# Optimization experiments

Measured on AMD Instinct MI355X. Metric: run time of the kernel, lower is better.

Reference implementation:

```python
import jax, jax.numpy as jnp
import numpy as np

B, S, D, H, DK, DV = 4, 2048, 512, 8, 64, 64
LN_EPS = 1e-5


def setup_inputs() -> dict:
    key = jax.random.key(0)
    ks = jax.random.split(key, 8)
    scale = 1.0 / np.sqrt(D)
    return {
        "input_Q": jax.random.normal(ks[0], (B, S, D), jnp.float32),
        "input_K": jax.random.normal(ks[1], (B, S, D), jnp.float32),
        "input_V": jax.random.normal(ks[2], (B, S, D), jnp.float32),
        "attn_mask": jax.random.randint(ks[3], (B, S, S), 0, 2).astype(jnp.bool_),
        "W_Q": jax.random.normal(ks[4], (D, H * DK), jnp.float32) * scale,
        "W_K": jax.random.normal(ks[5], (D, H * DK), jnp.float32) * scale,
        "W_V": jax.random.normal(ks[6], (D, H * DV), jnp.float32) * scale,
        "W_fc": jax.random.normal(ks[7], (H * DV, D), jnp.float32) * scale,
        "ln_gamma": jnp.ones((D,), jnp.float32),
        "ln_beta": jnp.zeros((D,), jnp.float32),
    }


def reference(input_Q, input_K, input_V, attn_mask, W_Q, W_K, W_V, W_fc, ln_gamma, ln_beta):
    b, s, _ = input_Q.shape
    # projections -> [b, h, s, d]
    Q = (input_Q @ W_Q).reshape(b, s, H, DK).transpose(0, 2, 1, 3)
    K = (input_K @ W_K).reshape(b, s, H, DK).transpose(0, 2, 1, 3)
    V = (input_V @ W_V).reshape(b, s, H, DV).transpose(0, 2, 1, 3)
    # full [b, h, q, k] score matrix (faithful to explicit matmul->mask->softmax)
    scores = jnp.einsum("bhqd,bhkd->bhqk", Q, K) / np.sqrt(DK).astype(np.float32)
    scores = jnp.where(attn_mask[:, None, :, :], -jnp.inf, scores)
    attn = jax.nn.softmax(scores, axis=-1)
    context = jnp.einsum("bhqk,bhkd->bhqd", attn, V)  # [b, h, s, dv]
    context = context.transpose(0, 2, 1, 3).reshape(b, s, H * DV)
    output = context @ W_fc  # dropout is identity in eval / p=0
    x = output + input_Q  # residual
    mean = jnp.mean(x, axis=-1, keepdims=True)
    var = jnp.var(x, axis=-1, keepdims=True)
    return (x - mean) * jax.lax.rsqrt(var + LN_EPS) * ln_gamma + ln_beta
```

## Files before the change

### kernel.cpp

```cpp
#include <hip/hip_runtime.h>


#define B_ 4
#define S_ 2048
#define D_ 512
#define H_ 8

typedef __attribute__((ext_vector_type(8))) short short8_t;
typedef __attribute__((ext_vector_type(4))) short short4_t;
typedef __attribute__((ext_vector_type(4))) float f32x4;
typedef __attribute__((ext_vector_type(16))) float f32x16;
typedef __attribute__((ext_vector_type(4))) unsigned u32x4;
typedef __attribute__((ext_vector_type(2))) unsigned u32x2;

__device__ __forceinline__ short f2bf(float f) {
    unsigned u = __builtin_bit_cast(unsigned, f);
    u += 0x7fff + ((u >> 16) & 1);
    return (short)(u >> 16);
}

__device__ __forceinline__ unsigned pk2(float a, float b) {
    return __builtin_amdgcn_perm(__builtin_bit_cast(unsigned, b),
                                 __builtin_bit_cast(unsigned, a), 0x07060302u);
}

__device__ __forceinline__ float bflo(unsigned u) {
    return __builtin_bit_cast(float, u << 16);
}
__device__ __forceinline__ float bfhi(unsigned u) {
    return __builtin_bit_cast(float, u & 0xffff0000u);
}

__global__ __launch_bounds__(256) void pack_mask_kernel(const void* __restrict__ mask,
                                                        unsigned* __restrict__ bits) {
    __shared__ int isBool;
    if (threadIdx.x == 0) isBool = 0;
    __syncthreads();
    const unsigned char* bytes = (const unsigned char*)mask;
    if (threadIdx.x < 64) {
        if (bytes[threadIdx.x * 4 + 1] | bytes[threadIdx.x * 4 + 2] | bytes[threadIdx.x * 4 + 3])
            isBool = 1;
    }
    __syncthreads();
    int t = blockIdx.x * 256 + threadIdx.x;
    int half = t & 1, q = (t >> 1) & 2047, kt = (t >> 12) & 31, b = t >> 17;
    size_t src = ((size_t)(b * 2048 + q)) * 2048 + kt * 64 + half * 32;
    unsigned v = 0;
    if (isBool) {
        const unsigned char* p = bytes + src;
        #pragma unroll
        for (int i = 0; i < 32; ++i) v |= (p[i] ? 1u : 0u) << i;
    } else {
        const int* p = (const int*)mask + src;
        #pragma unroll
        for (int i = 0; i < 32; ++i) v |= (p[i] ? 1u : 0u) << i;
    }
    bits[(((size_t)(b * 32 + kt)) * 2048 + q) * 2 + half] = ~v;
}

__global__ __launch_bounds__(256) void proj_kernel(
    const float* __restrict__ inQ, const float* __restrict__ inK, const float* __restrict__ inV,
    const float* __restrict__ wq, const float* __restrict__ wk, const float* __restrict__ wv,
    short* __restrict__ Qp, short* __restrict__ Kp, short* __restrict__ Vp) {
    __shared__ short As[64 * 64];
    __shared__ short Bs[64 * 64];
    const int z = blockIdx.z;
    const float* A = (z == 0) ? inQ : ((z == 1) ? inK : inV);
    const float* W = (z == 0) ? wq : ((z == 1) ? wk : wv);
    short* O = (z == 0) ? Qp : ((z == 1) ? Kp : Vp);
    const float scale = (z == 0) ? 0.125f * 1.44269504f : 1.0f;
    const int bm = blockIdx.x * 64, bn = blockIdx.y * 64;
    const int tid = threadIdx.x, lane = tid & 63, wv_ = tid >> 6;
    const int wm = (wv_ >> 1) * 32, wn = (wv_ & 1) * 32;
    f32x4 acc[2][2] = {};

    for (int k0 = 0; k0 < 512; k0 += 64) {
        __syncthreads();
        #pragma unroll
        for (int it = 0; it < 4; ++it) {
            int g = tid + it * 256;
            int r = g >> 4, c4 = (g & 15) * 4;
            f32x4 v = *(const f32x4*)(A + (size_t)(bm + r) * 512 + k0 + c4);
            u32x2 u = { pk2(v.x, v.y), pk2(v.z, v.w) };
            *(u32x2*)((char*)As + r * 128 + ((c4 * 2) ^ ((r & 7) << 4))) = u;
        }
        #pragma unroll
        for (int it = 0; it < 2; ++it) {
            int g = tid + it * 256;
            int kp = g >> 4, n4 = (g & 15) * 4;
            const float* wrow = W + (size_t)(k0 + 2 * kp) * 512 + bn + n4;
            f32x4 va = *(const f32x4*)(wrow);
            f32x4 vb = *(const f32x4*)(wrow + 512);
            #pragma unroll
            for (int j = 0; j < 4; ++j) {
                int n = n4 + j;
                *(unsigned*)((char*)Bs + n * 128 + ((4 * kp) ^ ((n & 7) << 4))) = pk2(va[j], vb[j]);
            }
        }
        __syncthreads();
        #pragma unroll
        for (int kk = 0; kk < 2; ++kk) {
            short8_t af[2], bfr[2];
            #pragma unroll
            for (int rf = 0; rf < 2; ++rf) {
                int row = wm + rf * 16 + (lane & 15);
                af[rf] = *(const short8_t*)((const char*)As + row * 128 +
                          ((kk * 64 + ((lane >> 4) * 16)) ^ ((row & 7) << 4)));
            }
            #pragma unroll
            for (int cf = 0; cf < 2; ++cf) {
                int n = wn + cf * 16 + (lane & 15);
                bfr[cf] = *(const short8_t*)((const char*)Bs + n * 128 +
                           ((kk * 64 + ((lane >> 4) * 16)) ^ ((n & 7) << 4)));
            }
            __builtin_amdgcn_s_setprio(1);
            #pragma unroll
            for (int rf = 0; rf < 2; ++rf)
                #pragma unroll
                for (int cf = 0; cf < 2; ++cf)
                    acc[rf][cf] = __builtin_amdgcn_mfma_f32_16x16x32_bf16(af[rf], bfr[cf], acc[rf][cf], 0, 0, 0);
            __builtin_amdgcn_s_setprio(0);
        }
    }

    if (z == 0) {
        #pragma unroll
        for (int rf = 0; rf < 2; ++rf)
            #pragma unroll
            for (int cf = 0; cf < 2; ++cf)
                #pragma unroll
                for (int r = 0; r < 4; ++r) {
                    int row = bm + wm + rf * 16 + (lane >> 4) * 4 + r;
                    int col = bn + wn + cf * 16 + (lane & 15);
                    size_t idx = ((((size_t)(row >> 11)) * 8 + (col >> 6)) * 2048 + (row & 2047)) * 64 + (col & 63);
                    O[idx] = f2bf(acc[rf][cf][r] * scale);
                }
    } else {
        const int bb = bm >> 11, kt = (bm & 2047) >> 6, hh = bn >> 6;
        const size_t base = ((size_t)(bb * 8 + hh)) * 131072 + (size_t)kt * 4096;
        __syncthreads();
        if (z == 1) {
            #pragma unroll
            for (int rf = 0; rf < 2; ++rf)
                #pragma unroll
                for (int cf = 0; cf < 2; ++cf)
                    #pragma unroll
                    for (int r = 0; r < 4; ++r) {
                        int key = wm + rf * 16 + (lane >> 4) * 4 + r;
                        int dk = wn + cf * 16 + (lane & 15);
                        *(short*)((char*)As + key * 128 + ((dk * 2) ^ ((key & 7) << 4))) = f2bf(acc[rf][cf][r]);
                    }
        } else {
            #pragma unroll
            for (int rf = 0; rf < 2; ++rf)
                #pragma unroll
                for (int cf = 0; cf < 2; ++cf)
                    #pragma unroll
                    for (int r = 0; r < 4; ++r) {
                        int key = wm + rf * 16 + (lane >> 4) * 4 + r;
                        int dv = wn + cf * 16 + (lane & 15);
                        *(short*)((char*)As + dv * 128 + ((key * 2) ^ ((dv & 7) << 4))) = f2bf(acc[rf][cf][r]);
                    }
        }
        __syncthreads();
        #pragma unroll
        for (int it = 0; it < 2; ++it) {
            int u = tid + it * 256;
            int blk = u >> 7, h2 = (u >> 6) & 1, rr = u & 63;
            short8_t v8 = *(const short8_t*)((const char*)As + rr * 128 +
                           ((blk * 32 + h2 * 16) ^ ((rr & 7) << 4)));
            *(short8_t*)(O + base + (size_t)u * 8) = v8;
        }
    }
}

template<int NSPLIT>
__global__ __launch_bounds__(256, 4) void attn_kernel(
    const short* __restrict__ Qp, const short* __restrict__ Kf, const short* __restrict__ Vf,
    const unsigned long long* __restrict__ mbits64, short* __restrict__ ctx,
    short* __restrict__ pO, float* __restrict__ pL) {
    __shared__ short Pw_all[4][2048];
    int flat = blockIdx.x + 16 * (blockIdx.y + 8 * NSPLIT * blockIdx.z);
    int x8 = flat & 7, s = flat >> 3;
    int group = x8 * (4 * NSPLIT) + (s >> 4);
    int qi = s & 15;
    int bh = group / NSPLIT, kvh = group % NSPLIT;
    const int b = bh >> 3, h = bh & 7;
    const int tid = threadIdx.x, lane = tid & 63, w = tid >> 6;
    const int hi = lane >> 5, r31 = lane & 31;
    const size_t hb = ((size_t)(b * 8 + h)) * 131072;
    const int qw = qi * 128 + w * 32;
    const int q_lane = qw + r31;
    const int NT = 32 / NSPLIT;
    const int t_beg = kvh * NT, t_end = t_beg + NT;

    short8_t qf[4];
    #pragma unroll
    for (int ks = 0; ks < 4; ++ks)
        qf[ks] = *(const short8_t*)(Qp + hb + (size_t)q_lane * 64 + ks * 16 + hi * 8);

    const short* Kb_ = Kf + hb + hi * 512 + r31 * 8;
    const short* Vb_ = Vf + hb + hi * 512 + r31 * 8;
    const unsigned long long* mrow = mbits64 + (size_t)b * 65536 + q_lane;

    f32x16 o0 = {}, o1 = {};
    float l_run = 0.f;

    for (int kt = t_beg; kt < t_end; ++kt) {
        const short* kp = Kb_ + (size_t)kt * 4096;
        unsigned long long wmx = mrow[(size_t)kt * 2048] >> (hi * 4);
        unsigned kl = (unsigned)wmx, kh = (unsigned)(wmx >> 32);

        f32x16 s0 = {}, s1 = {};
        __builtin_amdgcn_s_setprio(1);
        #pragma unroll
        for (int ks = 0; ks < 4; ++ks) {
            short8_t kf0 = *(const short8_t*)(kp + ks * 1024);
            short8_t kf1 = *(const short8_t*)(kp + ks * 1024 + 256);
            s0 = __builtin_amdgcn_mfma_f32_32x32x16_bf16(kf0, qf[ks], s0, 0, 0, 0);
            s1 = __builtin_amdgcn_mfma_f32_32x32x16_bf16(kf1, qf[ks], s1, 0, 0, 0);
        }
        __builtin_amdgcn_s_setprio(0);

        float r4[4] = { 0.f, 0.f, 0.f, 0.f };
        #pragma unroll
        for (int reg = 0; reg < 16; ++reg) {
            const int pos = (reg >> 2) * 8 + (reg & 3);
            float e0 = __builtin_amdgcn_exp2f(s0[reg]);
            float e1 = __builtin_amdgcn_exp2f(s1[reg]);
            unsigned k0b = (unsigned)__builtin_amdgcn_sbfe((int)kl, pos, 1);
            unsigned k1b = (unsigned)__builtin_amdgcn_sbfe((int)kh, pos, 1);
            float v0 = __builtin_bit_cast(float, __builtin_bit_cast(unsigned, e0) & k0b);
            float v1 = __builtin_bit_cast(float, __builtin_bit_cast(unsigned, e1) & k1b);
            s0[reg] = v0; s1[reg] = v1;
            r4[reg & 3] += v0 + v1;
        }
        float rs = (r4[0] + r4[1]) + (r4[2] + r4[3]);
        rs += __shfl_xor(rs, 32, 64);
        l_run += rs;

        const short* vp = Vb_ + (size_t)kt * 4096;
        #pragma unroll
        for (int kb = 0; kb < 4; ++kb) {
            const int e = (kb & 1) * 8;
            unsigned c0 = (kb < 2) ? pk2(s0[e + 0], s0[e + 1]) : pk2(s1[e + 0], s1[e + 1]);
            unsigned c1 = (kb < 2) ? pk2(s0[e + 2], s0[e + 3]) : pk2(s1[e + 2], s1[e + 3]);
            unsigned c2 = (kb < 2) ? pk2(s0[e + 4], s0[e + 5]) : pk2(s1[e + 4], s1[e + 5]);
            unsigned c3 = (kb < 2) ? pk2(s0[e + 6], s0[e + 7]) : pk2(s1[e + 6], s1[e + 7]);
#if __has_builtin(__builtin_amdgcn_permlane32_swap)
            u32x2 r02 = __builtin_amdgcn_permlane32_swap(c0, c2, false, false);
            u32x2 r13 = __builtin_amdgcn_permlane32_swap(c1, c3, false, false);
            u32x4 bw = { r02[0], r13[0], r02[1], r13[1] };
#else
            unsigned x0 = __shfl_xor(c0, 32, 64), x1 = __shfl_xor(c1, 32, 64);
            unsigned x2 = __shfl_xor(c2, 32, 64), x3 = __shfl_xor(c3, 32, 64);
            unsigned w0 = hi ? x2 : c0, w1 = hi ? x3 : c1;
            unsigned w2 = hi ? c2 : x0, w3 = hi ? c3 : x1;
            u32x4 bw = { w0, w1, w2, w3 };
#endif
            short8_t pb = __builtin_bit_cast(short8_t, bw);
            short8_t vf0 = *(const short8_t*)(vp + kb * 1024);
            short8_t vf1 = *(const short8_t*)(vp + kb * 1024 + 256);
            __builtin_amdgcn_s_setprio(1);
            o0 = __builtin_amdgcn_mfma_f32_32x32x16_bf16(vf0, pb, o0, 0, 0, 0);
            o1 = __builtin_amdgcn_mfma_f32_32x32x16_bf16(vf1, pb, o1, 0, 0, 0);
            __builtin_amdgcn_s_setprio(0);
        }
    }

    float invl = 1.0f / fmaxf(l_run, 1e-37f);
    short* Pw = Pw_all[w];
    #pragma unroll
    for (int dvb = 0; dvb < 2; ++dvb)
        #pragma unroll
        for (int g = 0; g < 4; ++g) {
            short4_t v4;
            #pragma unroll
            for (int t = 0; t < 4; ++t) {
                float val = (dvb ? o1[g * 4 + t] : o0[g * 4 + t]) * invl;
                v4[t] = f2bf(val);
            }
            int dv0 = dvb * 32 + g * 8 + hi * 4;
            *(short4_t*)((char*)Pw + r31 * 128 + ((dv0 * 2) ^ ((r31 & 7) << 4))) = v4;
        }
    asm volatile("s_waitcnt lgkmcnt(0)" ::: "memory");
    if (NSPLIT > 1) {
        const size_t bhn = (size_t)(bh * NSPLIT + kvh);
        #pragma unroll
        for (int c = 0; c < 4; ++c) {
            int idx = c * 64 + lane;
            int qq = idx >> 3, ch = idx & 7;
            short8_t rowv = *(const short8_t*)((const char*)Pw + qq * 128 + ((ch * 16) ^ ((qq & 7) << 4)));
            *(short8_t*)(pO + (bhn * 2048 + qw + qq) * 64 + ch * 8) = rowv;
        }
        if (lane < 32) pL[bhn * 2048 + q_lane] = l_run;
    } else {
        #pragma unroll
        for (int c = 0; c < 4; ++c) {
            int idx = c * 64 + lane;
            int qq = idx >> 3, ch = idx & 7;
            short8_t rowv = *(const short8_t*)((const char*)Pw + qq * 128 + ((ch * 16) ^ ((qq & 7) << 4)));
            *(short8_t*)(ctx + ((size_t)(b * 2048 + qw + qq)) * 512 + h * 64 + ch * 8) = rowv;
        }
    }
}

template<int NSPLIT>
__global__ __launch_bounds__(256) void combine_kernel(
    const short* __restrict__ pO, const float* __restrict__ pL,
    short* __restrict__ ctx) {
    const int row = blockIdx.x;
    const int b = row >> 11, q = row & 2047;
    const int e0 = threadIdx.x * 2;
    const int h = e0 >> 6, dv = e0 & 63;
    const size_t base = ((size_t)((b * 8 + h) * NSPLIT)) * 2048 + q;
    float wsum = 0.f, r0 = 0.f, r1 = 0.f;
    #pragma unroll
    for (int i = 0; i < NSPLIT; ++i) {
        float wv = pL[base + (size_t)i * 2048];
        unsigned a = *(const unsigned*)(pO + (base + (size_t)i * 2048) * 64 + dv);
        wsum += wv;
        r0 += bflo(a) * wv;
        r1 += bfhi(a) * wv;
    }
    float inv = 1.f / fmaxf(wsum, 1e-37f);
    *(unsigned*)(ctx + (size_t)row * 512 + e0) = pk2(r0 * inv, r1 * inv);
}

__global__ __launch_bounds__(256) void fc_kernel(
    const short* __restrict__ ctx, const float* __restrict__ wfc,
    const float* __restrict__ inQ, float* __restrict__ xbuf) {
    __shared__ short As[64 * 64];
    __shared__ short Bs[64 * 64];
    const int bm = blockIdx.x * 64, bn = blockIdx.y * 64;
    const int tid = threadIdx.x, lane = tid & 63, wv_ = tid >> 6;
    const int wm = (wv_ >> 1) * 32, wn = (wv_ & 1) * 32;
    f32x4 acc[2][2] = {};

    for (int k0 = 0; k0 < 512; k0 += 64) {
        __syncthreads();
        #pragma unroll
        for (int it = 0; it < 2; ++it) {
            int g = tid + it * 256;
            int r = g >> 3, c8 = (g & 7) * 8;
            short8_t v = *(const short8_t*)(ctx + (size_t)(bm + r) * 512 + k0 + c8);
            *(short8_t*)((char*)As + r * 128 + ((c8 * 2) ^ ((r & 7) << 4))) = v;
        }
        #pragma unroll
        for (int it = 0; it < 2; ++it) {
            int g = tid + it * 256;
            int kp = g >> 4, n4 = (g & 15) * 4;
            const float* wrow = wfc + (size_t)(k0 + 2 * kp) * 512 + bn + n4;
            f32x4 va = *(const f32x4*)(wrow);
            f32x4 vb = *(const f32x4*)(wrow + 512);
            #pragma unroll
            for (int j = 0; j < 4; ++j) {
                int n = n4 + j;
                *(unsigned*)((char*)Bs + n * 128 + ((4 * kp) ^ ((n & 7) << 4))) = pk2(va[j], vb[j]);
            }
        }
        __syncthreads();
        #pragma unroll
        for (int kk = 0; kk < 2; ++kk) {
            short8_t af[2], bfr[2];
            #pragma unroll
            for (int rf = 0; rf < 2; ++rf) {
                int row = wm + rf * 16 + (lane & 15);
                af[rf] = *(const short8_t*)((const char*)As + row * 128 +
                          ((kk * 64 + ((lane >> 4) * 16)) ^ ((row & 7) << 4)));
            }
            #pragma unroll
            for (int cf = 0; cf < 2; ++cf) {
                int n = wn + cf * 16 + (lane & 15);
                bfr[cf] = *(const short8_t*)((const char*)Bs + n * 128 +
                           ((kk * 64 + ((lane >> 4) * 16)) ^ ((n & 7) << 4)));
            }
            __builtin_amdgcn_s_setprio(1);
            #pragma unroll
            for (int rf = 0; rf < 2; ++rf)
                #pragma unroll
                for (int cf = 0; cf < 2; ++cf)
                    acc[rf][cf] = __builtin_amdgcn_mfma_f32_16x16x32_bf16(af[rf], bfr[cf], acc[rf][cf], 0, 0, 0);
            __builtin_amdgcn_s_setprio(0);
        }
    }
    #pragma unroll
    for (int rf = 0; rf < 2; ++rf)
        #pragma unroll
        for (int cf = 0; cf < 2; ++cf)
            #pragma unroll
            for (int r = 0; r < 4; ++r) {
                int row = bm + wm + rf * 16 + (lane >> 4) * 4 + r;
                int col = bn + wn + cf * 16 + (lane & 15);
                size_t idx = (size_t)row * 512 + col;
                xbuf[idx] = acc[rf][cf][r] + inQ[idx];
            }
}

__global__ __launch_bounds__(256) void ln_kernel(
    const float* __restrict__ x, const float* __restrict__ gamma,
    const float* __restrict__ beta, float* __restrict__ out) {
    __shared__ float rs[4], rq[4];
    const int row = blockIdx.x, tid = threadIdx.x;
    const int w = tid >> 6, lane = tid & 63;
    float2 v = *(const float2*)(x + (size_t)row * 512 + tid * 2);
    float s = v.x + v.y, sq = v.x * v.x + v.y * v.y;
    #pragma unroll
    for (int off = 32; off; off >>= 1) {
        s += __shfl_down(s, off, 64);
        sq += __shfl_down(sq, off, 64);
    }
    if (lane == 0) { rs[w] = s; rq[w] = sq; }
    __syncthreads();
    if (tid == 0) {
        rs[0] = rs[0] + rs[1] + rs[2] + rs[3];
        rq[0] = rq[0] + rq[1] + rq[2] + rq[3];
    }
    __syncthreads();
    float mean = rs[0] * (1.f / 512.f);
    float var = rq[0] * (1.f / 512.f) - mean * mean;
    float inv = rsqrtf(var + 1e-5f);
    int c0 = tid * 2;
    float2 g = *(const float2*)(gamma + c0);
    float2 be = *(const float2*)(beta + c0);
    float2 o;
    o.x = (v.x - mean) * inv * g.x + be.x;
    o.y = (v.y - mean) * inv * g.y + be.y;
    *(float2*)(out + (size_t)row * 512 + c0) = o;
}

extern "C" void kernel_launch(void* const* d_in, const int* in_sizes, int n_in,
                              void* d_out, int out_size, void* d_ws, size_t ws_size,
                              hipStream_t stream) {
    const float* inQ = (const float*)d_in[0];
    const float* inK = (const float*)d_in[1];
    const float* inV = (const float*)d_in[2];
    const void* mask = d_in[3];
    const float* wq = (const float*)d_in[4];
    const float* wk = (const float*)d_in[5];
    const float* wv = (const float*)d_in[6];
    const float* wfc = (const float*)d_in[7];
    const float* gamma = (const float*)d_in[8];
    const float* beta = (const float*)d_in[9];
    float* out = (float*)d_out;
    char* ws = (char*)d_ws;

    short* Qp = (short*)(ws);
    short* Kp = (short*)(ws + (size_t)(8 << 20));
    short* Vp = (short*)(ws + (size_t)(16 << 20));
    short* ctx = (short*)(ws + (size_t)(24 << 20));
    unsigned* mbits = (unsigned*)(ws + (size_t)(32 << 20));
    float* xbuf = (float*)(ws);

    short* pO = (short*)(ws + 35651584ull);
    float* pL = (float*)(ws + 35651584ull + 16777216ull);

    const bool split2 = ws_size >= 53477376ull;

    pack_mask_kernel<<<2048, 256, 0, stream>>>(mask, mbits);
    proj_kernel<<<dim3(128, 8, 3), 256, 0, stream>>>(inQ, inK, inV, wq, wk, wv, Qp, Kp, Vp);
    if (split2) {
        attn_kernel<2><<<dim3(16, 16, 4), 256, 0, stream>>>(
            Qp, Kp, Vp, (const unsigned long long*)mbits, ctx, pO, pL);
        combine_kernel<2><<<8192, 256, 0, stream>>>(pO, pL, ctx);
    } else {
        attn_kernel<1><<<dim3(16, 8, 4), 256, 0, stream>>>(
            Qp, Kp, Vp, (const unsigned long long*)mbits, ctx, pO, pL);
    }
    fc_kernel<<<dim3(128, 8, 1), 256, 0, stream>>>(ctx, wfc, inQ, xbuf);
    ln_kernel<<<8192, 256, 0, stream>>>(xbuf, gamma, beta, out);
}
```

Before: 142.8 us.

## Split KV across waves within block and combine in LDS, drop combine kernel

Each attention block now handles 32 queries, and its four waves each process a quarter of the key tiles. The wave results are merged in shared memory using the per-row softmax sums. This removes the separate global split-KV pass (partial output writes, the combine kernel launch and its re-reads) and gives more blocks. In exchange each block reloads Q per wave, gets less K/V reuse across queries, and adds a block-wide barrier plus an LDS reduction.

```diff
diff --git a/kernel.cpp b/kernel.cpp
--- a/kernel.cpp
+++ b/kernel.cpp
@@ -24,11 +24,8 @@
                                  __builtin_bit_cast(unsigned, a), 0x07060302u);
 }
 
-__device__ __forceinline__ float bflo(unsigned u) {
-    return __builtin_bit_cast(float, u << 16);
-}
-__device__ __forceinline__ float bfhi(unsigned u) {
-    return __builtin_bit_cast(float, u & 0xffff0000u);
+__device__ __forceinline__ float bf2f(short v) {
+    return __builtin_bit_cast(float, (unsigned)((unsigned short)v) << 16);
 }
 
 __global__ __launch_bounds__(256) void pack_mask_kernel(const void* __restrict__ mask,
@@ -174,25 +171,22 @@
     }
 }
 
-template<int NSPLIT>
 __global__ __launch_bounds__(256, 4) void attn_kernel(
     const short* __restrict__ Qp, const short* __restrict__ Kf, const short* __restrict__ Vf,
-    const unsigned long long* __restrict__ mbits64, short* __restrict__ ctx,
-    short* __restrict__ pO, float* __restrict__ pL) {
+    const unsigned long long* __restrict__ mbits64, short* __restrict__ ctx) {
     __shared__ short Pw_all[4][2048];
-    int flat = blockIdx.x + 16 * (blockIdx.y + 8 * NSPLIT * blockIdx.z);
+    __shared__ float l_lds[4][32];
+    int flat = blockIdx.x + 64 * (blockIdx.y + 8 * blockIdx.z);
     int x8 = flat & 7, s = flat >> 3;
-    int group = x8 * (4 * NSPLIT) + (s >> 4);
-    int qi = s & 15;
-    int bh = group / NSPLIT, kvh = group % NSPLIT;
+    int bh = x8 * 4 + (s >> 6);
+    int qi = s & 63;
     const int b = bh >> 3, h = bh & 7;
     const int tid = threadIdx.x, lane = tid & 63, w = tid >> 6;
     const int hi = lane >> 5, r31 = lane & 31;
-    const size_t hb = ((size_t)(b * 8 + h)) * 131072;
-    const int qw = qi * 128 + w * 32;
+    const size_t hb = ((size_t)bh) * 131072;
+    const int qw = qi * 32;
     const int q_lane = qw + r31;
-    const int NT = 32 / NSPLIT;
-    const int t_beg = kvh * NT, t_end = t_beg + NT;
+    const int t_beg = w * 8, t_end = t_beg + 8;
 
     short8_t qf[4];
     #pragma unroll
@@ -283,48 +277,26 @@
             int dv0 = dvb * 32 + g * 8 + hi * 4;
             *(short4_t*)((char*)Pw + r31 * 128 + ((dv0 * 2) ^ ((r31 & 7) << 4))) = v4;
         }
-    asm volatile("s_waitcnt lgkmcnt(0)" ::: "memory");
-    if (NSPLIT > 1) {
-        const size_t bhn = (size_t)(bh * NSPLIT + kvh);
-        #pragma unroll
-        for (int c = 0; c < 4; ++c) {
-            int idx = c * 64 + lane;
-            int qq = idx >> 3, ch = idx & 7;
-            short8_t rowv = *(const short8_t*)((const char*)Pw + qq * 128 + ((ch * 16) ^ ((qq & 7) << 4)));
-            *(short8_t*)(pO + (bhn * 2048 + qw + qq) * 64 + ch * 8) = rowv;
-        }
-        if (lane < 32) pL[bhn * 2048 + q_lane] = l_run;
-    } else {
-        #pragma unroll
-        for (int c = 0; c < 4; ++c) {
-            int idx = c * 64 + lane;
-            int qq = idx >> 3, ch = idx & 7;
-            short8_t rowv = *(const short8_t*)((const char*)Pw + qq * 128 + ((ch * 16) ^ ((qq & 7) << 4)));
-            *(short8_t*)(ctx + ((size_t)(b * 2048 + qw + qq)) * 512 + h * 64 + ch * 8) = rowv;
-        }
-    }
-}
-
-template<int NSPLIT>
-__global__ __launch_bounds__(256) void combine_kernel(
-    const short* __restrict__ pO, const float* __restrict__ pL,
-    short* __restrict__ ctx) {
-    const int row = blockIdx.x;
-    const int b = row >> 11, q = row & 2047;
-    const int e0 = threadIdx.x * 2;
-    const int h = e0 >> 6, dv = e0 & 63;
-    const size_t base = ((size_t)((b * 8 + h) * NSPLIT)) * 2048 + q;
-    float wsum = 0.f, r0 = 0.f, r1 = 0.f;
+    if (hi == 0) l_lds[w][r31] = l_run;
+    __syncthreads();
+
+    const int q = tid >> 3, j = tid & 7;
+    float acc8[8] = {};
+    float wsum = 0.f;
     #pragma unroll
-    for (int i = 0; i < NSPLIT; ++i) {
-        float wv = pL[base + (size_t)i * 2048];
-        unsigned a = *(const unsigned*)(pO + (base + (size_t)i * 2048) * 64 + dv);
-        wsum += wv;
-        r0 += bflo(a) * wv;
-        r1 += bfhi(a) * wv;
+    for (int ww = 0; ww < 4; ++ww) {
+        float lw = l_lds[ww][q];
+        wsum += lw;
+        short8_t v8 = *(const short8_t*)((const char*)Pw_all[ww] + q * 128 + ((j * 16) ^ ((q & 7) << 4)));
+        #pragma unroll
+        for (int e = 0; e < 8; ++e)
+            acc8[e] += bf2f(v8[e]) * lw;
     }
     float inv = 1.f / fmaxf(wsum, 1e-37f);
-    *(unsigned*)(ctx + (size_t)row * 512 + e0) = pk2(r0 * inv, r1 * inv);
+    u32x4 ov = { pk2(acc8[0] * inv, acc8[1] * inv), pk2(acc8[2] * inv, acc8[3] * inv),
+                 pk2(acc8[4] * inv, acc8[5] * inv), pk2(acc8[6] * inv, acc8[7] * inv) };
+    *(short8_t*)(ctx + ((size_t)(b * 2048 + qw + q)) * 512 + h * 64 + j * 8) =
+        __builtin_bit_cast(short8_t, ov);
 }
 
 __global__ __launch_bounds__(256) void fc_kernel(
@@ -452,21 +424,10 @@
     unsigned* mbits = (unsigned*)(ws + (size_t)(32 << 20));
     float* xbuf = (float*)(ws);
 
-    short* pO = (short*)(ws + 35651584ull);
-    float* pL = (float*)(ws + 35651584ull + 16777216ull);
-
-    const bool split2 = ws_size >= 53477376ull;
-
     pack_mask_kernel<<<2048, 256, 0, stream>>>(mask, mbits);
     proj_kernel<<<dim3(128, 8, 3), 256, 0, stream>>>(inQ, inK, inV, wq, wk, wv, Qp, Kp, Vp);
-    if (split2) {
-        attn_kernel<2><<<dim3(16, 16, 4), 256, 0, stream>>>(
-            Qp, Kp, Vp, (const unsigned long long*)mbits, ctx, pO, pL);
-        combine_kernel<2><<<8192, 256, 0, stream>>>(pO, pL, ctx);
-    } else {
-        attn_kernel<1><<<dim3(16, 8, 4), 256, 0, stream>>>(
-            Qp, Kp, Vp, (const unsigned long long*)mbits, ctx, pO, pL);
-    }
+    attn_kernel<<<dim3(64, 8, 4), 256, 0, stream>>>(
+        Qp, Kp, Vp, (const unsigned long long*)mbits, ctx);
     fc_kernel<<<dim3(128, 8, 1), 256, 0, stream>>>(ctx, wfc, inQ, xbuf);
     ln_kernel<<<8192, 256, 0, stream>>>(xbuf, gamma, beta, out);
 }
```

Measured after the change: 139.3 us. -2.4%, faster.
